# Performance work log

Hardware: AMD Instinct MI355X
Metric: run time of the kernel (lower is better)

## Reference

```python
import jax, jax.numpy as jnp
import numpy as np

T, N, C, D, S = 512, 32, 1296, 512, 30
NORM_SCALE = 32.0
NEGINF = -1e9


def setup_inputs() -> dict:
    key = jax.random.key(0)
    k1, k2, k3, k4, k5 = jax.random.split(key, 5)
    feats = jax.random.normal(k1, (T * N, D), dtype=jnp.float32)
    classifier_weight = jax.random.normal(k2, (D, C), dtype=jnp.float32)
    labeling = jax.random.randint(k3, (N, S), 1, C)  # targets cannot be blank(0)
    logit_lgts = (T - jax.random.randint(k4, (N,), 0, 32)).astype(jnp.int32)
    labeling_lgts = (S - jax.random.randint(k5, (N,), 0, 5)).astype(jnp.int32)
    return dict(feats=feats, classifier_weight=classifier_weight,
                labeling=labeling, logit_lgts=logit_lgts, labeling_lgts=labeling_lgts)


def _ctc_loss(log_probs, labels, in_lens, lab_lens):
    # log_probs: (T, N, C); labels: (N, S); blank = 0; reduction = 'sum'
    Tt, Nn, Cc = log_probs.shape
    Ss = labels.shape[1]
    L = 2 * Ss + 1
    # extended labeling: blank, l1, blank, l2, ..., blank  -> (N, L)
    ext = jnp.zeros((Nn, L), dtype=labels.dtype).at[:, 1::2].set(labels)
    # gather per-state log-probs: (T, N, L)
    lp_ext = jnp.take_along_axis(log_probs, jnp.broadcast_to(ext[None], (Tt, Nn, L)), axis=2)
    # skip transition s-2 -> s allowed iff s > 1 and ext[s] != ext[s-2]
    skip_ok = jnp.concatenate(
        [jnp.zeros((Nn, 2), dtype=bool), ext[:, 2:] != ext[:, :-2]], axis=1)
    alpha0 = (jnp.full((Nn, L), NEGINF, dtype=log_probs.dtype)
              .at[:, 0].set(lp_ext[0, :, 0])
              .at[:, 1].set(lp_ext[0, :, 1]))

    def step(alpha, inp):
        lp_t, t = inp  # lp_t: (N, L)
        a1 = alpha
        a2 = jnp.pad(alpha[:, :-1], ((0, 0), (1, 0)), constant_values=NEGINF)
        a3 = jnp.where(skip_ok,
                       jnp.pad(alpha[:, :-2], ((0, 0), (2, 0)), constant_values=NEGINF),
                       NEGINF)
        new = jax.nn.logsumexp(jnp.stack([a1, a2, a3], axis=0), axis=0) + lp_t
        # freeze alpha once t reaches a sample's input length
        alpha = jnp.where((t < in_lens)[:, None], new, alpha)
        return alpha, None

    alpha, _ = jax.lax.scan(step, alpha0, (lp_ext[1:], jnp.arange(1, Tt)))
    Ln = 2 * lab_lens + 1  # (N,)
    last = jnp.take_along_axis(alpha, (Ln - 1)[:, None], axis=1)[:, 0]
    last2 = jnp.take_along_axis(alpha, (Ln - 2)[:, None], axis=1)[:, 0]
    nll = -jnp.logaddexp(last, last2)
    return jnp.sum(nll)


def reference(feats, classifier_weight, labeling, logit_lgts, labeling_lgts):
    # RadialCTC: cosine logits with norm_scale, then CTC on log-softmax.
    w_n = classifier_weight / jnp.linalg.norm(classifier_weight, axis=0, keepdims=True)  # (D, C)
    f_n = feats / jnp.linalg.norm(feats, axis=1, keepdims=True)  # (T*N, D)
    logits = NORM_SCALE * (f_n @ w_n)  # (T*N, C)
    log_probs = jax.nn.log_softmax(logits.reshape(T, N, C), axis=-1)
    return _ctc_loss(log_probs, labeling, logit_lgts, labeling_lgts)
```

## Files before the change

### kernel.cpp

```cpp
#include <hip/hip_runtime.h>
#include <stdint.h>
#include <stddef.h>


typedef _Float16 f16;
typedef _Float16 f16x8 __attribute__((ext_vector_type(8)));
typedef float f32x4 __attribute__((ext_vector_type(4)));
typedef __attribute__((address_space(1))) void* as1_void_ptr;
typedef __attribute__((address_space(3))) void* as3_void_ptr;

#define TT 512
#define NN 32
#define CC 1296
#define DD 512
#define SS 30
#define CP 1408
#define LL 61
#define NORM_SCALE 32.0f
#define LOG2E 1.4426950408889634f
#define LN2   0.6931471805599453f

#define PREP_WBLK (CP / 16)
#define PREP_ZBLK 16
#define PREP_FBLK (TT * NN / 4)

#define GEMM_BLK ((TT * NN / 128) * (CP / 128))
#define MEGA_GC  NN
#define MEGA_BLK (MEGA_GC + GEMM_BLK)

__device__ __forceinline__ float fexp2(float x) { return __builtin_amdgcn_exp2f(x); }
__device__ __forceinline__ float flog2(float x) { return __builtin_amdgcn_logf(x); }

__device__ __forceinline__ double dpp_sr1_zero64(double x) {
    long long b = __double_as_longlong(x);
    int lo = (int)(b & 0xFFFFFFFFLL);
    int hi = (int)(b >> 32);
    int lo2 = __builtin_amdgcn_update_dpp(0, lo, 0x138, 0xF, 0xF, false);
    int hi2 = __builtin_amdgcn_update_dpp(0, hi, 0x138, 0xF, 0xF, false);
    return __longlong_as_double(((long long)hi2 << 32) |
                                (unsigned long long)(unsigned int)lo2);
}
template <int CTRL>
__device__ __forceinline__ int dpp_imax_level(int m) {
    int t = __builtin_amdgcn_update_dpp(0, m, CTRL, 0xF, 0xF, false);
    return m > t ? m : t;
}

__global__ __launch_bounds__(256) void prep_kernel(const float* __restrict__ W,
                                                   const float* __restrict__ feats,
                                                   f16* __restrict__ wt,
                                                   f16* __restrict__ fn,
                                                   float* __restrict__ sumexp) {
    int bx = blockIdx.x, tid = threadIdx.x;
    if (bx < PREP_WBLK) {
        __shared__ float red[256];
        __shared__ float rqs[16];
        int c0 = bx * 16;
        int cl = tid & 15, dg = tid >> 4;
        int c = c0 + cl;
        float ss = 0.f;
        if (c < CC) {
            for (int d = dg; d < DD; d += 16) {
                float v = W[(size_t)d * CC + c];
                ss += v * v;
            }
        }
        red[tid] = ss;
        __syncthreads();
        if (tid < 16) {
            float s2 = 0.f;
            #pragma unroll
            for (int k = 0; k < 16; ++k) s2 += red[tid + 16 * k];
            rqs[tid] = rsqrtf(s2);
        }
        __syncthreads();
        int c_loc = tid >> 4, dl = tid & 15;
        int cc = c0 + c_loc;
        float rq = rqs[c_loc];
        #pragma unroll 4
        for (int it = 0; it < 32; ++it) {
            int d = dl + it * 16;
            float v = (cc < CC) ? W[(size_t)d * CC + cc] * rq : 0.f;
            wt[(size_t)cc * DD + d] = (f16)v;
        }
    } else if (bx < PREP_WBLK + PREP_ZBLK) {
        int zb = bx - PREP_WBLK;
        float4 z = {0.f, 0.f, 0.f, 0.f};
        ((float4*)sumexp)[zb * 256 + tid] = z;
    } else {
        int fb = bx - PREP_WBLK - PREP_ZBLK;
        int wv = (fb * 256 + tid) >> 6;
        int lane = tid & 63;
        const float4* src = (const float4*)(feats + (size_t)wv * DD) + lane * 2;
        float4 a = src[0], b = src[1];
        float ss = a.x*a.x + a.y*a.y + a.z*a.z + a.w*a.w
                 + b.x*b.x + b.y*b.y + b.z*b.z + b.w*b.w;
        #pragma unroll
        for (int off = 32; off; off >>= 1) ss += __shfl_xor(ss, off);
        float r = rsqrtf(ss);
        f16x8 o;
        o[0]=(f16)(a.x*r); o[1]=(f16)(a.y*r); o[2]=(f16)(a.z*r); o[3]=(f16)(a.w*r);
        o[4]=(f16)(b.x*r); o[5]=(f16)(b.y*r); o[6]=(f16)(b.z*r); o[7]=(f16)(b.w*r);
        *(f16x8*)(fn + (size_t)wv * DD + lane * 8) = o;
    }
}

template <int NT>
__device__ __forceinline__ void gather_wave(const f16* __restrict__ A,
                                            const f16* __restrict__ B,
                                            const int* __restrict__ labels,
                                            float* __restrict__ lp_lab,
                                            int n, int rbase, int lane) {
    int lm = lane & 15, hi = lane >> 4;
    int cls0 = (lm == 0) ? 0 : labels[n * SS + lm - 1];
    int cls1 = (lm >= 15) ? 0 : labels[n * SS + lm + 15];
    const f16* pb0 = B + (size_t)cls0 * DD + hi * 8;
    const f16* pb1 = B + (size_t)cls1 * DD + hi * 8;
    const f16* pa0 = A + ((size_t)(rbase + lm) * NN + n) * DD + hi * 8;
    for (int c = 0; c < 4; ++c) {
        f32x4 acc[NT][2];
        #pragma unroll
        for (int i = 0; i < NT; ++i) {
            acc[i][0] = (f32x4){0.f, 0.f, 0.f, 0.f};
            acc[i][1] = (f32x4){0.f, 0.f, 0.f, 0.f};
        }
        const f16* pac = pa0 + (size_t)c * 128 * NN * DD;
        for (int kb = 0; kb < 16; ++kb) {
            f16x8 bf0 = *(const f16x8*)(pb0 + kb * 32);
            f16x8 bf1 = *(const f16x8*)(pb1 + kb * 32);
            #pragma unroll
            for (int i = 0; i < NT; ++i) {
                f16x8 af = *(const f16x8*)(pac + (size_t)(i * 16) * NN * DD + kb * 32);
                acc[i][0] = __builtin_amdgcn_mfma_f32_16x16x32_f16(af, bf0, acc[i][0], 0, 0, 0);
                acc[i][1] = __builtin_amdgcn_mfma_f32_16x16x32_f16(af, bf1, acc[i][1], 0, 0, 0);
            }
        }
        #pragma unroll
        for (int i = 0; i < NT; ++i) {
            #pragma unroll
            for (int jn = 0; jn < 2; ++jn) {
                int jc = jn * 16 + lm;
                if (jc >= 31) continue;
                float4 o;
                o.x = acc[i][jn][0] * (NORM_SCALE * LOG2E);
                o.y = acc[i][jn][1] * (NORM_SCALE * LOG2E);
                o.z = acc[i][jn][2] * (NORM_SCALE * LOG2E);
                o.w = acc[i][jn][3] * (NORM_SCALE * LOG2E);
                *(float4*)&lp_lab[((size_t)n * 31 + jc) * TT
                                  + c * 128 + rbase + i * 16 + hi * 4] = o;
            }
        }
        __syncthreads();
    }
}

__global__ __launch_bounds__(256) void mega_kernel(const f16* __restrict__ A,
                                                   const f16* __restrict__ B,
                                                   const int* __restrict__ labels,
                                                   const int* __restrict__ in_lens,
                                                   const int* __restrict__ lab_lens,
                                                   float* __restrict__ sumexp,
                                                   float* __restrict__ lp_lab,
                                                   double* __restrict__ part) {
    __shared__ __align__(16) f16 sm[8192];
    int bx = blockIdx.x;
    int tid = threadIdx.x;
    int w = tid >> 6, lane = tid & 63;
    int lm = lane & 15, hi = lane >> 4;
    int sw = (lm >> 1) & 3;

    if (bx >= MEGA_GC) {
        int j = bx - MEGA_GC;
        int bm = j & 127, bn = j >> 7;
        int wm = w >> 1, wn = w & 1;
        f32x4 acc[4][4];
        f32x4 zero = {0.f, 0.f, 0.f, 0.f};
        #pragma unroll
        for (int i = 0; i < 4; ++i)
            #pragma unroll
            for (int jj = 0; jj < 4; ++jj) acc[i][jj] = zero;

        for (int kb = 0; kb < 16; ++kb) {
            #pragma unroll
            for (int p = 0; p < 2; ++p) {
                int s = p * 256 + tid;
                int row = s >> 2;
                int ch = (s & 3) ^ ((row >> 1) & 3);
                const f16* ga = A + (size_t)(bm * 128 + row) * DD + kb * 32 + ch * 8;
                const f16* gb = B + (size_t)(bn * 128 + row) * DD + kb * 32 + ch * 8;
                __builtin_amdgcn_global_load_lds((as1_void_ptr)ga,
                    (as3_void_ptr)&sm[(p * 256 + w * 64) * 8], 16, 0, 0);
                __builtin_amdgcn_global_load_lds((as1_void_ptr)gb,
                    (as3_void_ptr)&sm[4096 + (p * 256 + w * 64) * 8], 16, 0, 0);
            }
            __syncthreads();
            f16x8 af[4], bf[4];
            #pragma unroll
            for (int i = 0; i < 4; ++i)
                af[i] = *(const f16x8*)&sm[(wm * 64 + i * 16 + lm) * 32 + (hi ^ sw) * 8];
            #pragma unroll
            for (int jj = 0; jj < 4; ++jj)
                bf[jj] = *(const f16x8*)&sm[4096 + (wn * 64 + jj * 16 + lm) * 32 + (hi ^ sw) * 8];
            #pragma unroll
            for (int i = 0; i < 4; ++i)
                #pragma unroll
                for (int jj = 0; jj < 4; ++jj)
                    acc[i][jj] = __builtin_amdgcn_mfma_f32_16x16x32_f16(af[i], bf[jj], acc[i][jj], 0, 0, 0);
            __syncthreads();
        }
        #pragma unroll
        for (int i = 0; i < 4; ++i) {
            float rs[4] = {0.f, 0.f, 0.f, 0.f};
            #pragma unroll
            for (int jj = 0; jj < 4; ++jj) {
                int c = bn * 128 + wn * 64 + jj * 16 + lm;
                bool ok = (c < CC);
                #pragma unroll
                for (int r = 0; r < 4; ++r)
                    rs[r] += ok ? fexp2(acc[i][jj][r] * (NORM_SCALE * LOG2E)) : 0.f;
            }
            #pragma unroll
            for (int off = 1; off < 16; off <<= 1) {
                #pragma unroll
                for (int r = 0; r < 4; ++r) rs[r] += __shfl_xor(rs[r], off);
            }
            if (lm == 0) {
                int rowb = bm * 128 + wm * 64 + i * 16 + hi * 4;
                #pragma unroll
                for (int r = 0; r < 4; ++r) atomicAdd(&sumexp[rowb + r], rs[r]);
            }
        }
        return;
    }

    int n = bx;
    if (w > 0) {
        if (w < 3) gather_wave<3>(A, B, labels, lp_lab, n, (w - 1) * 48, lane);
        else       gather_wave<2>(A, B, labels, lp_lab, n, 96, lane);
        return;
    }

    int s = lane;
    bool valid = s < LL;
    int ext = (valid && (s & 1)) ? labels[n * SS + (s >> 1)] : 0;
    int jmap = (valid && (s & 1)) ? ((s >> 1) + 1) : 0;
    int ext2 = __shfl_up(ext, 2);
    double skipd = ((s >= 2) && valid && (ext != ext2)) ? 1.0 : 0.0;
    int Tin = in_lens[n];
    const float4* g4 = (const float4*)(lp_lab + ((size_t)n * 31 + jmap) * TT);

    __syncthreads();
    float4 cur = g4[0];
    float4 nxt = g4[1];
    float4 nx2 = g4[2];
    double beta = (s <= 1) ? (double)fexp2(cur.x) : 0.0;
    int Mi = 0;

    auto stepL = [&](float lp) {
        double P = (double)fexp2(lp);
        double b1 = dpp_sr1_zero64(beta);
        double b2 = dpp_sr1_zero64(b1);
        beta = (beta + b1 + b2 * skipd) * P;
    };
    auto renorm = [&]() {
        int h = (int)(__double_as_longlong(beta) >> 32);
        h = dpp_imax_level<0x111>(h);
        h = dpp_imax_level<0x112>(h);
        h = dpp_imax_level<0x114>(h);
        h = dpp_imax_level<0x118>(h);
        int r0 = __builtin_amdgcn_readlane(h, 15);
        int r1 = __builtin_amdgcn_readlane(h, 31);
        int r2 = __builtin_amdgcn_readlane(h, 47);
        int r3 = __builtin_amdgcn_readlane(h, 63);
        int mx = max(max(r0, r1), max(r2, r3));
        int e11 = mx >> 20;
        double scale = __longlong_as_double((long long)(2046 - e11) << 52);
        beta *= scale;
        Mi += e11 - 1023;
    };

    stepL(cur.y); stepL(cur.z); stepL(cur.w);
    renorm();
    int remaining = Tin - 4;
    int g = 1;
    for (int c = 0; c < 4; ++c) {
        if (c > 0) {
            __syncthreads();
            nxt = g4[g];
            nx2 = g4[g + 1];
        }
        int gend = 32 * (c + 1);
        while (g < gend && remaining >= 4) {
            cur = nxt; nxt = nx2;
            int gi = g + 2; if (gi > 127) gi = 127;
            nx2 = g4[gi];
            stepL(cur.x); stepL(cur.y); stepL(cur.z); stepL(cur.w);
            renorm();
            remaining -= 4; ++g;
        }
    }
    cur = nxt;
    if (remaining > 0) stepL(cur.x);
    if (remaining > 1) stepL(cur.y);
    if (remaining > 2) stepL(cur.z);

    int Ln = 2 * lab_lens[n] + 1;
    double last  = __shfl(beta, Ln - 1);
    double last2 = __shfl(beta, Ln - 2);
    double smv = last + last2;
    long long bb = __double_as_longlong(smv);
    int e = (int)(bb >> 52) - 1023;
    double mant = __longlong_as_double((bb & 0xFFFFFFFFFFFFFLL) | (1023LL << 52));
    if (s == 0)
        part[n] = (double)flog2((float)mant) + (double)(e + Mi);
}

__global__ __launch_bounds__(1024) void final_kernel(const float* __restrict__ sumexp,
                                                     const int* __restrict__ in_lens,
                                                     const double* __restrict__ part,
                                                     float* __restrict__ out) {
    int tid = threadIdx.x;
    int v = tid >> 6, lane = tid & 63;
    __shared__ float nl[NN];
    #pragma unroll
    for (int k = 0; k < 2; ++k) {
        int n = v * 2 + k;
        int Tin = in_lens[n];
        double ms = 0.0;
        for (int t = lane; t < Tin; t += 64)
            ms += (double)flog2(sumexp[(size_t)t * NN + n]);
        #pragma unroll
        for (int off = 32; off; off >>= 1) ms += __shfl_xor(ms, off);
        if (lane == 0) nl[n] = (float)(-(part[n] - ms) * LN2);
    }
    __syncthreads();
    if (tid == 0) {
        float t = 0.f;
        for (int i = 0; i < NN; ++i) t += nl[i];
        out[0] = t;
    }
}

extern "C" void kernel_launch(void* const* d_in, const int* in_sizes, int n_in,
                              void* d_out, int out_size, void* d_ws, size_t ws_size,
                              hipStream_t stream) {
    const float* feats        = (const float*)d_in[0];
    const float* W            = (const float*)d_in[1];
    const int*   labeling     = (const int*)d_in[2];
    const int*   logit_lgts   = (const int*)d_in[3];
    const int*   labeling_lgts= (const int*)d_in[4];
    float* out = (float*)d_out;
    char* ws = (char*)d_ws;

    size_t off = 0;
    f16*   wt     = (f16*)(ws + off);   off += (size_t)CP * DD * 2;
    f16*   fn     = (f16*)(ws + off);   off += (size_t)TT * NN * DD * 2;
    float* sumexp = (float*)(ws + off); off += (size_t)TT * NN * 4;
    float* lp_lab = (float*)(ws + off); off += (size_t)NN * 31 * TT * 4;
    double* part  = (double*)(ws + off); off += NN * 8;

    prep_kernel<<<PREP_WBLK + PREP_ZBLK + PREP_FBLK, 256, 0, stream>>>(
        W, feats, wt, fn, sumexp);
    mega_kernel<<<MEGA_BLK, 256, 0, stream>>>(fn, wt, labeling, logit_lgts,
                                              labeling_lgts, sumexp, lp_lab, part);
    final_kernel<<<1, 1024, 0, stream>>>(sumexp, logit_lgts, part, out);

    (void)in_sizes; (void)n_in; (void)out_size; (void)ws_size;
}
```

Measured before the change: 163.1 us.

## Fuse two CTC alpha steps per update and raise wave priority on recursion

Replaces the single-timestep CTC recursion with a two-step composite update. Precomputed shifted skip masks let beta advance two timesteps using four shifted copies of beta, which shortens the serial dependency chain of DPP shifts and multiplies. Prefetching moves to 8-timestep groups with renormalization every 8 steps instead of every 4, and the recursion wave runs at raised scheduling priority. In exchange it does more FLOPs per step, uses more registers, and lets the double-precision values grow over longer spans between renorms.

```diff
diff --git a/kernel.cpp b/kernel.cpp
--- a/kernel.cpp
+++ b/kernel.cpp
@@ -246,14 +246,13 @@
     int jmap = (valid && (s & 1)) ? ((s >> 1) + 1) : 0;
     int ext2 = __shfl_up(ext, 2);
     double skipd = ((s >= 2) && valid && (ext != ext2)) ? 1.0 : 0.0;
+    double sk1 = dpp_sr1_zero64(skipd);
+    double sk2 = dpp_sr1_zero64(sk1);
+    double kk2 = skipd * sk2;
     int Tin = in_lens[n];
     const float4* g4 = (const float4*)(lp_lab + ((size_t)n * 31 + jmap) * TT);
 
-    __syncthreads();
-    float4 cur = g4[0];
-    float4 nxt = g4[1];
-    float4 nx2 = g4[2];
-    double beta = (s <= 1) ? (double)fexp2(cur.x) : 0.0;
+    double beta = 0.0;
     int Mi = 0;
 
     auto stepL = [&](float lp) {
@@ -261,6 +260,23 @@
         double b1 = dpp_sr1_zero64(beta);
         double b2 = dpp_sr1_zero64(b1);
         beta = (beta + b1 + b2 * skipd) * P;
+    };
+    auto step2 = [&](float lp1, float lp2) {
+        double q  = (double)fexp2(lp1);
+        double P2 = (double)fexp2(lp2);
+        double q1 = dpp_sr1_zero64(q);
+        double q2 = dpp_sr1_zero64(q1);
+        double c1 = q + q1;
+        double c2 = fma(skipd, q + q2, q1);
+        double c3 = fma(sk1, q1, skipd * q2);
+        double c4 = kk2 * q2;
+        double b1 = dpp_sr1_zero64(beta);
+        double b2 = dpp_sr1_zero64(b1);
+        double b3 = dpp_sr1_zero64(b2);
+        double b4 = dpp_sr1_zero64(b3);
+        double u = fma(c1, b1, q * beta);
+        double v = fma(c3, b3, c2 * b2);
+        beta = (u + fma(c4, b4, v)) * P2;
     };
     auto renorm = [&]() {
         int h = (int)(__double_as_longlong(beta) >> 32);
@@ -279,30 +295,44 @@
         Mi += e11 - 1023;
     };
 
-    stepL(cur.y); stepL(cur.z); stepL(cur.w);
+    __builtin_amdgcn_s_setprio(1);
+    __syncthreads();
+    float4 a0 = g4[0], a1 = g4[1];
+    float4 pc0 = g4[2], pc1 = g4[3];
+    float4 pn0 = g4[4], pn1 = g4[5];
+    beta = (s <= 1) ? (double)fexp2(a0.x) : 0.0;
+
+    stepL(a0.y); stepL(a0.z); stepL(a0.w);
+    stepL(a1.x); stepL(a1.y); stepL(a1.z); stepL(a1.w);
     renorm();
-    int remaining = Tin - 4;
-    int g = 1;
+    int remaining = Tin - 8;
+    int g = 2;
     for (int c = 0; c < 4; ++c) {
         if (c > 0) {
             __syncthreads();
-            nxt = g4[g];
-            nx2 = g4[g + 1];
+            pc0 = g4[g];     pc1 = g4[g + 1];
+            pn0 = g4[g + 2]; pn1 = g4[g + 3];
         }
         int gend = 32 * (c + 1);
-        while (g < gend && remaining >= 4) {
-            cur = nxt; nxt = nx2;
-            int gi = g + 2; if (gi > 127) gi = 127;
-            nx2 = g4[gi];
-            stepL(cur.x); stepL(cur.y); stepL(cur.z); stepL(cur.w);
+        while (g + 2 <= gend && remaining >= 8) {
+            int i0 = g + 4 > 127 ? 127 : g + 4;
+            int i1 = g + 5 > 127 ? 127 : g + 5;
+            float4 pp0 = g4[i0], pp1 = g4[i1];
+            step2(pc0.x, pc0.y); step2(pc0.z, pc0.w);
+            step2(pc1.x, pc1.y); step2(pc1.z, pc1.w);
             renorm();
-            remaining -= 4; ++g;
-        }
-    }
-    cur = nxt;
-    if (remaining > 0) stepL(cur.x);
-    if (remaining > 1) stepL(cur.y);
-    if (remaining > 2) stepL(cur.z);
+            pc0 = pn0; pc1 = pn1; pn0 = pp0; pn1 = pp1;
+            remaining -= 8; g += 2;
+        }
+    }
+    if (remaining > 0) stepL(pc0.x);
+    if (remaining > 1) stepL(pc0.y);
+    if (remaining > 2) stepL(pc0.z);
+    if (remaining > 3) stepL(pc0.w);
+    if (remaining > 4) stepL(pc1.x);
+    if (remaining > 5) stepL(pc1.y);
+    if (remaining > 6) stepL(pc1.z);
+    __builtin_amdgcn_s_setprio(0);
 
     int Ln = 2 * lab_lens[n] + 1;
     double last  = __shfl(beta, Ln - 1);
```

After: 154.2 us. 5.5% less time.
